# Optimization experiments

Measured on AMD Instinct MI355X. Metric: run time of the kernel, lower is better.

## Reference

```python
import jax, jax.numpy as jnp
import numpy as np

NSAMPLE = 16   # knn neighbors for cost volume
KCLUST = 8     # cluster size stand-in for custom_cluster_pc1 (min_count=8)
B, N, D = 2, 4096, 64


def _sqdist(src, dst):
    # src [B,N,C], dst [B,M,C] -> [B,N,M]
    d = (jnp.sum(src * src, -1)[:, :, None]
         + jnp.sum(dst * dst, -1)[:, None, :]
         - 2.0 * jnp.einsum('bnc,bmc->bnm', src, dst))
    return jnp.maximum(d, 0.0)


def _knn(k, xyz, new_xyz):
    return jax.lax.top_k(-_sqdist(new_xyz, xyz), k)[1]  # [B,S,k] indices of k smallest


def _group(points, idx):
    # points [B,M,C], idx [B,N,K] -> [B,N,K,C]
    b = jnp.arange(points.shape[0])[:, None, None]
    return points[b, idx]


def _weightnet(x, w1, b1, w2, b2, w3, b3):
    # x [B,N,K,3]; 1x1 conv stack == per-point MLP, relu
    h = jax.nn.relu(jnp.einsum('bnkc,cd->bnkd', x, w1) + b1)
    h = jax.nn.relu(jnp.einsum('bnkc,cd->bnkd', h, w2) + b2)
    return jax.nn.relu(jnp.einsum('bnkc,cd->bnkd', h, w3) + b3)


def _leaky(x):
    return jnp.where(x > 0, x, 0.1 * x)


def _forward(xyz1, xyz2, points1, points2, vel1, vel2, mask1, mask2,
             w_xyz, w_vel, w_points,
             mlp_w1, mlp_b1, mlp_w2, mlp_b2,
             wn1_w1, wn1_b1, wn1_w2, wn1_b2, wn1_w3, wn1_b3,
             wn2_w1, wn2_b1, wn2_w2, wn2_b2, wn2_w3, wn2_b3):
    xyz1t = jnp.transpose(xyz1, (0, 2, 1))      # [B,N1,3]
    xyz2t = jnp.transpose(xyz2, (0, 2, 1))      # [B,N2,3]
    p1t = jnp.transpose(points1, (0, 2, 1))     # [B,N1,D1]
    p2t = jnp.transpose(points2, (0, 2, 1))     # [B,N2,D2]

    # --- custom_cluster_pc1 stand-in: knn clusters of pc1 with its velocities ---
    idx_c = _knn(KCLUST, xyz1t, xyz1t)                     # [B,N,KC]
    cc = _group(xyz1t, idx_c)                              # [B,N,KC,3]
    cv = _group(vel1[..., None], idx_c)[..., 0]            # [B,N,KC]

    u = cc / jnp.linalg.norm(cc, axis=-1, keepdims=True)
    ATA = jnp.einsum('bnki,bnkj->bnij', u, u) + 1e-6 * jnp.eye(3, dtype=u.dtype)
    ATb = jnp.einsum('bnki,bnk->bni', u, cv)
    v_world = jnp.linalg.solve(ATA, ATb[..., None])[..., 0]  # [B,N,3]

    # --- feature-space knn between weighted (xyz, points) concatenations ---
    f1 = jnp.concatenate([w_xyz * xyz1t, w_points * p1t], axis=-1)
    f2 = jnp.concatenate([w_xyz * xyz2t, w_points * p2t], axis=-1)
    knn_idx = _knn(NSAMPLE, f2, f1)                        # [B,N1,K]

    neighbor_xyz = _group(xyz2t, knn_idx)                  # [B,N1,K,3]
    direction_xyz = neighbor_xyz - xyz1t[:, :, None, :]
    g2 = _group(p2t, knn_idx)                              # [B,N1,K,D2]
    g1 = jnp.broadcast_to(p1t[:, :, None, :], g2.shape[:3] + (p1t.shape[-1],))
    new_points = jnp.concatenate([g1, g2, direction_xyz], axis=-1)  # [B,N1,K,D1+D2+3]

    h = _leaky(jnp.einsum('bnkc,cd->bnkd', new_points, mlp_w1) + mlp_b1)
    h = _leaky(jnp.einsum('bnkc,cd->bnkd', h, mlp_w2) + mlp_b2)    # [B,N1,K,128]

    w = _weightnet(direction_xyz, wn1_w1, wn1_b1, wn1_w2, wn1_b2, wn1_w3, wn1_b3)
    point_to_patch = jnp.sum(w * h, axis=2)                # [B,N1,128]

    # --- second grouping in rigid-velocity space ---
    idx2 = _knn(NSAMPLE, v_world, v_world)
    nxyz1 = _group(xyz1t, idx2)
    dir2 = nxyz1 - xyz1t[:, :, None, :]
    w2 = _weightnet(dir2, wn2_w1, wn2_b1, wn2_w2, wn2_b2, wn2_w3, wn2_b3)
    gcost = _group(point_to_patch, idx2)                   # [B,N1,K,128]
    patch_to_patch = jnp.sum(w2 * gcost, axis=2)           # [B,N1,128]

    return jnp.transpose(patch_to_patch, (0, 2, 1)), v_world  # [B,128,N1], [B,N1,3]


def setup_inputs() -> dict:
    key = jax.random.key(0)
    ks = jax.random.split(key, 24)
    s = 0.05
    inp = {
        'xyz1': jax.random.normal(ks[0], (B, 3, N), jnp.float32),
        'xyz2': jax.random.normal(ks[1], (B, 3, N), jnp.float32),
        'points1': jax.random.normal(ks[2], (B, D, N), jnp.float32),
        'points2': jax.random.normal(ks[3], (B, D, N), jnp.float32),
        'vel1': jax.random.normal(ks[4], (B, N), jnp.float32),
        'vel2': jax.random.normal(ks[5], (B, N), jnp.float32),
        'mask1': jnp.ones((B, N), jnp.float32),
        'mask2': jnp.ones((B, N), jnp.float32),
        'w_xyz': jnp.float32(0.4), 'w_vel': jnp.float32(0.2), 'w_points': jnp.float32(0.4),
        'mlp_w1': jax.random.normal(ks[6], (2 * D + 3, 128), jnp.float32) * s,
        'mlp_b1': jnp.zeros((128,), jnp.float32),
        'mlp_w2': jax.random.normal(ks[7], (128, 128), jnp.float32) * s,
        'mlp_b2': jnp.zeros((128,), jnp.float32),
    }
    for tag, base in (('wn1', 8), ('wn2', 14)):
        inp[f'{tag}_w1'] = jax.random.normal(ks[base], (3, 8), jnp.float32) * s
        inp[f'{tag}_b1'] = jnp.zeros((8,), jnp.float32)
        inp[f'{tag}_w2'] = jax.random.normal(ks[base + 1], (8, 8), jnp.float32) * s
        inp[f'{tag}_b2'] = jnp.zeros((8,), jnp.float32)
        inp[f'{tag}_w3'] = jax.random.normal(ks[base + 2], (8, 128), jnp.float32) * s
        inp[f'{tag}_b3'] = jnp.zeros((128,), jnp.float32)
    return inp


def reference(xyz1, xyz2, points1, points2, vel1, vel2, mask1, mask2,
              w_xyz, w_vel, w_points,
              mlp_w1, mlp_b1, mlp_w2, mlp_b2,
              wn1_w1, wn1_b1, wn1_w2, wn1_b2, wn1_w3, wn1_b3,
              wn2_w1, wn2_b1, wn2_w2, wn2_b2, wn2_w3, wn2_b3):
    return _forward(xyz1, xyz2, points1, points2, vel1, vel2, mask1, mask2,
                    w_xyz, w_vel, w_points,
                    mlp_w1, mlp_b1, mlp_w2, mlp_b2,
                    wn1_w1, wn1_b1, wn1_w2, wn1_b2, wn1_w3, wn1_b3,
                    wn2_w1, wn2_b1, wn2_w2, wn2_b2, wn2_w3, wn2_b3)
```

## Files before the change

### kernel.cpp

```cpp
#include <hip/hip_runtime.h>

#define NPTS 4096
#define NQ   8192
#define DD   64
#define KNN  16
#define KC   8
#define NSEG3 32
#define NPSEG 32
#define KB96 96
#define FSTR 104
#define VOFF 1048576

#define ALWAYS_INLINE __attribute__((always_inline)) inline

typedef __attribute__((ext_vector_type(8))) short bf16x8;
typedef __attribute__((ext_vector_type(4))) float f32x4;

__device__ ALWAYS_INLINE float leakyf(float x) { return x > 0.f ? x : 0.1f * x; }

__device__ ALWAYS_INLINE unsigned short bf16rne(float f) {
  unsigned u = __float_as_uint(f);
  u = (u + 0x7FFFu + ((u >> 16) & 1u)) >> 16;
  return (unsigned short)u;
}

__device__ ALWAYS_INLINE float packdt(float d, unsigned tag12) {
  return __uint_as_float((__float_as_uint(d) & 0xFFFFF000u) | tag12);
}

#define TK8_FOREACH(M)  M(0) M(1) M(2) M(3) M(4) M(5) M(6) M(7)
#define TK16_FOREACH(M) M(0) M(1) M(2) M(3) M(4) M(5) M(6) M(7) \
                        M(8) M(9) M(10) M(11) M(12) M(13) M(14) M(15)

#define TK_DECL1(i) float tkd##i = 3.4e38f; int tki##i = 0;
#define TK_STEP1(i) { bool c = vd < tkd##i; float t_ = tkd##i; int u_ = tki##i; \
                      tkd##i = c ? vd : tkd##i; tki##i = c ? vi : tki##i; \
                      vd = c ? t_ : vd; vi = c ? u_ : vi; }
#define TK8_DECL  TK8_FOREACH(TK_DECL1)
#define TK8_INS(dexp, mexp)  { float vd = (dexp); int vi = (mexp); \
                               if (vd < tkd7)  { TK8_FOREACH(TK_STEP1) } }
#define TK8_RESET1(i) tkd##i = 3.4e38f; tki##i = 0;

#define PK_DECL1(i) float pk##i = __uint_as_float(0x7F7FFFFFu);
#define PK_RESET1(i) pk##i = __uint_as_float(0x7F7FFFFFu);
#define PK_STEP1(i) { float lo_ = fminf(pk##i, pv); pv = fmaxf(pk##i, pv); pk##i = lo_; }
#define PK16_DECL    TK16_FOREACH(PK_DECL1)
#define PK16_INS(ve) { float pv = (ve); TK16_FOREACH(PK_STEP1) }
#define PK_STORE1(i) pdq[i] = pk##i;
#define PK16_STORE   TK16_FOREACH(PK_STORE1)

__global__ __launch_bounds__(256) void k_prep(
    const float* __restrict__ xyz1, const float* __restrict__ xyz2,
    const float* __restrict__ pts1, const float* __restrict__ pts2,
    const float* __restrict__ w_xyz_p, const float* __restrict__ w_points_p,
    unsigned short* __restrict__ f1b, unsigned short* __restrict__ f2b,
    float* __restrict__ n1, float* __restrict__ n2a,
    float* __restrict__ p1t, float* __restrict__ p2t,
    float* __restrict__ x1t, float* __restrict__ x2t)
{
  __shared__ float s_acc[64][5];
  int tid = threadIdx.x;
  int nl = tid & 63, part = tid >> 6;
  int cloud = blockIdx.x >> 7;
  int gid = ((blockIdx.x & 127) << 6) + nl;
  int b = gid >> 12, n = gid & (NPTS - 1);
  float wx = w_xyz_p[0], wp = w_points_p[0];
  const float* xyz = cloud ? xyz2 : xyz1;
  const float* pts = cloud ? pts2 : pts1;
  unsigned short* fb = cloud ? f2b : f1b;
  float* nrm = cloud ? n2a : n1;
  float* pt  = cloud ? p2t : p1t;
  float* xt  = cloud ? x2t : x1t;
  const float* pb = pts + (size_t)b * DD * NPTS;
  float* pr = pt + (size_t)gid * DD;
  unsigned short* fr = fb + (size_t)gid * KB96;
  int c0 = part * 16;
  float acc = 0.f;
#pragma unroll 4
  for (int j = 0; j < 16; ++j) {
    float v = pb[(size_t)(c0 + j) * NPTS + n];
    pr[c0 + j] = v;
    float fv = wp * v;
    fr[3 + c0 + j] = bf16rne(fv);
    acc = fmaf(fv, fv, acc);
  }
  s_acc[nl][part] = acc;
  if (part == 1) { for (int c = 67; c < 82; ++c) fr[c] = 0; }
  else if (part == 2) { for (int c = 82; c < KB96; ++c) fr[c] = 0; }
  __syncthreads();
  if (part == 0) {
    const float* xb = xyz + (size_t)b * 3 * NPTS;
    float x = xb[n], y = xb[NPTS + n], z = xb[2 * NPTS + n];
    float nrm2 = fmaf(z, z, fmaf(y, y, x * x));
    float4 xv; xv.x = x; xv.y = y; xv.z = z; xv.w = nrm2;
    *(float4*)&xt[(size_t)gid * 4] = xv;
    float fx = wx * x, fy = wx * y, fz = wx * z;
    fr[0] = bf16rne(fx); fr[1] = bf16rne(fy); fr[2] = bf16rne(fz);
    float a = fmaf(fz, fz, fmaf(fy, fy, fx * fx));
    a += s_acc[nl][0] + s_acc[nl][1] + s_acc[nl][2] + s_acc[nl][3];
    nrm[gid] = a;
  }
}

__global__ __launch_bounds__(256) void k_knn3(
    const float* __restrict__ x4, float* __restrict__ pd, int* __restrict__ pi)
{
  __shared__ __align__(16) float4 sc[128];
  int seg = blockIdx.y;
  int Q = blockIdx.x * 256 + threadIdx.x;
  int b = Q >> 12;
  float4 q = *(const float4*)&x4[(size_t)Q * 4];
  TK8_DECL
  int gbase = (b << 12) + seg * 128;
  if (threadIdx.x < 128)
    sc[threadIdx.x] = *(const float4*)&x4[(size_t)(gbase + threadIdx.x) * 4];
  __syncthreads();
  int m0 = seg * 128;
#pragma unroll
  for (int j = 0; j < 128; ++j) {
    float4 c = sc[j];
    float dot = fmaf(q.z, c.z, fmaf(q.y, c.y, q.x * c.x));
    float d = fmaxf(q.w + c.w - 2.f * dot, 0.f);
    TK8_INS(d, m0 + j)
  }
  float* pdq = pd + ((size_t)Q * NSEG3 + seg) * 8;
  int* piq = pi + ((size_t)Q * NSEG3 + seg) * 8;
#define ST8(i) pdq[i] = tkd##i; piq[i] = tki##i;
  TK8_FOREACH(ST8)
#undef ST8
}

__global__ __launch_bounds__(256) void k_knnv(
    const float* __restrict__ x4, float* __restrict__ pd)
{
  __shared__ __align__(16) float4 sc[128];
  int seg = blockIdx.y;
  int Q = blockIdx.x * 256 + threadIdx.x;
  int b = Q >> 12;
  float4 q = *(const float4*)&x4[(size_t)Q * 4];
  PK16_DECL
  int gbase = (b << 12) + seg * 128;
  if (threadIdx.x < 128)
    sc[threadIdx.x] = *(const float4*)&x4[(size_t)(gbase + threadIdx.x) * 4];
  __syncthreads();
#pragma unroll
  for (int j = 0; j < 128; ++j) {
    float4 c = sc[j];
    float dot = fmaf(q.z, c.z, fmaf(q.y, c.y, q.x * c.x));
    float d = fmaxf(q.w + c.w - 2.f * dot, 0.f);
    PK16_INS(packdt(d, ((unsigned)j << 5) | (unsigned)seg))
  }
  float* pdq = pd + ((size_t)Q * NPSEG + seg) * 16;
  PK16_STORE
}

__global__ __launch_bounds__(256) void k_rigid(
    const float* __restrict__ pd, const int* __restrict__ pi,
    const float* __restrict__ x4, const float* __restrict__ vel1,
    float* __restrict__ vout, float* __restrict__ v4out)
{
  __shared__ __align__(16) float s_d[64][33];
  __shared__ __align__(16) int   s_i[64][33];
  int tid = threadIdx.x;
  int ql = tid >> 2, part = tid & 3;
  int Q = blockIdx.x * 64 + ql;
  int b = Q >> 12;
  TK8_DECL
  {
    int s0 = part * 8;
    const float* pbase = pd + ((size_t)Q * NSEG3 + s0) * 8;
    const int* ibase = pi + ((size_t)Q * NSEG3 + s0) * 8;
#pragma unroll
    for (int s = 0; s < 8; ++s) {
#pragma unroll
      for (int j = 0; j < 8; ++j) TK8_INS(pbase[s * 8 + j], ibase[s * 8 + j])
    }
  }
#define STP(i) s_d[ql][part * 8 + i] = tkd##i; s_i[ql][part * 8 + i] = tki##i;
  TK8_FOREACH(STP)
#undef STP
  __syncthreads();
  if (part != 0) return;
  TK8_FOREACH(TK8_RESET1)
#pragma unroll
  for (int j = 0; j < 32; ++j) TK8_INS(s_d[ql][j], s_i[ql][j])
  int base = b << 12;
  double a00 = 0, a01 = 0, a02 = 0, a11 = 0, a12 = 0, a22 = 0;
  double r0 = 0, r1 = 0, r2 = 0;
#define RIG_ACC(i) { \
    float4 c = *(const float4*)&x4[(size_t)(base + tki##i) * 4]; \
    float nr = sqrtf(c.w); \
    float ux = c.x / nr, uy = c.y / nr, uz = c.z / nr; \
    float cv = vel1[base + tki##i]; \
    double dx = ux, dy = uy, dz = uz, dvv = cv; \
    a00 += dx * dx; a01 += dx * dy; a02 += dx * dz; \
    a11 += dy * dy; a12 += dy * dz; a22 += dz * dz; \
    r0 += dx * dvv; r1 += dy * dvv; r2 += dz * dvv; }
  TK8_FOREACH(RIG_ACC)
#undef RIG_ACC
  a00 += 1e-6; a11 += 1e-6; a22 += 1e-6;
  double c00 = a11 * a22 - a12 * a12;
  double c01 = a02 * a12 - a01 * a22;
  double c02 = a01 * a12 - a02 * a11;
  double c11 = a00 * a22 - a02 * a02;
  double c12 = a02 * a01 - a00 * a12;
  double c22 = a00 * a11 - a01 * a01;
  double det = a00 * c00 + a01 * c01 + a02 * c02;
  double inv = 1.0 / det;
  float vx = (float)((c00 * r0 + c01 * r1 + c02 * r2) * inv);
  float vy = (float)((c01 * r0 + c11 * r1 + c12 * r2) * inv);
  float vz = (float)((c02 * r0 + c12 * r1 + c22 * r2) * inv);
  vout[(size_t)Q * 3 + 0] = vx;
  vout[(size_t)Q * 3 + 1] = vy;
  vout[(size_t)Q * 3 + 2] = vz;
  float4 v; v.x = vx; v.y = vy; v.z = vz;
  v.w = fmaf(vz, vz, fmaf(vy, vy, vx * vx));
  *(float4*)&v4out[(size_t)Q * 4] = v;
}

__global__ __launch_bounds__(256) void k_knnf_mfma(
    const unsigned short* __restrict__ f1b, const unsigned short* __restrict__ f2b,
    const float* __restrict__ n1, const float* __restrict__ n2a,
    float* __restrict__ pd)
{
  __shared__ __align__(16) unsigned short sf1[16 * FSTR];
  __shared__ __align__(16) unsigned short sf2[2][64 * FSTR];
  __shared__ __align__(16) float sn1[16];
  __shared__ __align__(16) float sn2[2][64];
  __shared__ __align__(16) float sD[64][17];
  int tid = threadIdx.x;
  int w = tid >> 6, lane = tid & 63;
  int i15 = lane & 15, g = lane >> 4, kr0 = g * 8;
  int blockq = blockIdx.x * 16;
  int b = blockq >> 12;
  int seg = blockIdx.y;
  int gbase = (b << 12) + seg * 2048;
  {
    const float4* src = (const float4*)(f1b + (size_t)blockq * KB96);
    if (tid < 192) ((float4*)sf1)[tid + tid / 12] = src[tid];
    if (tid < 16) sn1[tid] = n1[blockq + tid];
  }
  {
    const float4* src = (const float4*)(f2b + (size_t)gbase * KB96);
    int i0 = tid, i1 = tid + 256, i2 = tid + 512;
    ((float4*)sf2[0])[i0 + i0 / 12] = src[i0];
    ((float4*)sf2[0])[i1 + i1 / 12] = src[i1];
    ((float4*)sf2[0])[i2 + i2 / 12] = src[i2];
    if (tid < 64) sn2[0][tid] = n2a[gbase + tid];
  }
  __syncthreads();
  bf16x8 af0 = *(const bf16x8*)&sf1[i15 * FSTR + kr0];
  bf16x8 af1 = *(const bf16x8*)&sf1[i15 * FSTR + 32 + kr0];
  bf16x8 af2 = *(const bf16x8*)&sf1[i15 * FSTR + 64 + kr0];
  float nq0 = sn1[g * 4 + 0], nq1 = sn1[g * 4 + 1];
  float nq2 = sn1[g * 4 + 2], nq3 = sn1[g * 4 + 3];
  PK16_DECL
  int q_tk = tid & 15, p_tk = tid >> 4;
  for (int ch = 0; ch < 32; ++ch) {
    int cur = ch & 1;
    {
      int crow = w * 16 + i15;
      const unsigned short* c_ = &sf2[cur][crow * FSTR + kr0];
      f32x4 acc = {0.f, 0.f, 0.f, 0.f};
      acc = __builtin_amdgcn_mfma_f32_16x16x32_bf16(af0, *(const bf16x8*)&c_[0],  acc, 0, 0, 0);
      acc = __builtin_amdgcn_mfma_f32_16x16x32_bf16(af1, *(const bf16x8*)&c_[32], acc, 0, 0, 0);
      acc = __builtin_amdgcn_mfma_f32_16x16x32_bf16(af2, *(const bf16x8*)&c_[64], acc, 0, 0, 0);
      float nn2 = sn2[cur][crow];
      unsigned tag = (((unsigned)(ch * 4 + (crow & 3))) << 5) |
                     (unsigned)(seg * 16 + (crow >> 2));
      sD[crow][g * 4 + 0] = packdt(fmaxf(nq0 + nn2 - 2.f * acc[0], 0.f), tag);
      sD[crow][g * 4 + 1] = packdt(fmaxf(nq1 + nn2 - 2.f * acc[1], 0.f), tag);
      sD[crow][g * 4 + 2] = packdt(fmaxf(nq2 + nn2 - 2.f * acc[2], 0.f), tag);
      sD[crow][g * 4 + 3] = packdt(fmaxf(nq3 + nn2 - 2.f * acc[3], 0.f), tag);
    }
    __syncthreads();
    if (ch + 1 < 32) {
      const float4* src = (const float4*)(f2b + (size_t)(gbase + (ch + 1) * 64) * KB96);
      int i0 = tid, i1 = tid + 256, i2 = tid + 512;
      ((float4*)sf2[cur ^ 1])[i0 + i0 / 12] = src[i0];
      ((float4*)sf2[cur ^ 1])[i1 + i1 / 12] = src[i1];
      ((float4*)sf2[cur ^ 1])[i2 + i2 / 12] = src[i2];
      if (tid < 64) sn2[cur ^ 1][tid] = n2a[gbase + (ch + 1) * 64 + tid];
    }
#pragma unroll
    for (int j = 0; j < 4; ++j)
      PK16_INS(sD[p_tk * 4 + j][q_tk])
    __syncthreads();
  }
  int pseg = seg * 16 + p_tk;
  float* pdq = pd + ((size_t)(blockq + q_tk) * NPSEG + pseg) * 16;
  PK16_STORE
}

template<int MODE>
__global__ __launch_bounds__(256) void k_mergepk(
    const float* __restrict__ pd, int* __restrict__ oidx)
{
  __shared__ __align__(16) float s_k[64][65];
  int tid = threadIdx.x;
  int ql = tid >> 2, part = tid & 3;
  int Q = blockIdx.x * 64 + ql;
  PK16_DECL
  {
    const float* pbase = pd + ((size_t)Q * NPSEG + part * 8) * 16;
#pragma unroll
    for (int s = 0; s < 8; ++s) {
      for (int j = 0; j < 16; ++j) {
        float v = pbase[s * 16 + j];
        if (!(v < pk15)) break;
        PK16_INS(v)
      }
    }
  }
#define STK(i) s_k[ql][part * 16 + i] = pk##i;
  TK16_FOREACH(STK)
#undef STK
  __syncthreads();
  if (part != 0) return;
  TK16_FOREACH(PK_RESET1)
#pragma unroll
  for (int p = 0; p < 4; ++p) {
    for (int j = 0; j < 16; ++j) {
      float v = s_k[ql][p * 16 + j];
      if (!(v < pk15)) break;
      PK16_INS(v)
    }
  }
#define DEC(i) { unsigned u = __float_as_uint(pk##i); int m_; \
    unsigned ps = u & 31u, lo = (u >> 5) & 127u; \
    if (MODE == 0) m_ = (int)(((ps >> 4) << 11) + ((lo >> 2) << 6) + ((ps & 15u) << 2) + (lo & 3u)); \
    else m_ = (int)((ps << 7) + lo); \
    oidx[(size_t)Q * KNN + i] = m_; }
  TK16_FOREACH(DEC)
#undef DEC
}

#define PPB 8
__device__ ALWAYS_INLINE bf16x8 load_wfrag(const float* __restrict__ Wg,
                                           int kbase, int col, int kmax) {
  bf16x8 r;
#pragma unroll
  for (int j = 0; j < 8; ++j) {
    int k = kbase + j;
    float f = (k < kmax) ? Wg[(size_t)k * 128 + col] : 0.f;
    r[j] = (short)bf16rne(f);
  }
  return r;
}

__global__ __launch_bounds__(512) void k_mlp_mfma(
    const float* __restrict__ p1t, const float* __restrict__ p2t,
    const float* __restrict__ x1t, const float* __restrict__ x2t,
    const int* __restrict__ kidx,
    const float* __restrict__ W1, const float* __restrict__ B1v,
    const float* __restrict__ W2, const float* __restrict__ B2v,
    const float* __restrict__ wnw1, const float* __restrict__ wnb1,
    const float* __restrict__ wnw2, const float* __restrict__ wnb2,
    const float* __restrict__ wnw3, const float* __restrict__ wnb3,
    float* __restrict__ ptp)
{
  __shared__ __align__(16) unsigned short sA1[16 * 168];
  __shared__ __align__(16) unsigned short sH1[16 * 136];
  __shared__ __align__(16) float s_wv[16 * 128];
  __shared__ __align__(16) float s_c1[24];
  __shared__ __align__(16) float s_cb1[8];
  __shared__ __align__(16) float s_c2[64];
  __shared__ __align__(16) float s_cb2[8];
  __shared__ __align__(16) float s_w3[1024];
  __shared__ __align__(16) float s_b3[128];
  int tid = threadIdx.x;
  int w = tid >> 6, lane = tid & 63;
  int col = (w << 4) + (lane & 15);
  int kr0 = (lane >> 4) * 8;
  if (tid < 24) s_c1[tid] = wnw1[tid];
  else if (tid < 32) s_cb1[tid - 24] = wnb1[tid - 24];
  else if (tid < 96) s_c2[tid - 32] = wnw2[tid - 32];
  else if (tid < 104) s_cb2[tid - 96] = wnb2[tid - 96];
  if (tid >= 128 && tid < 256) s_b3[tid - 128] = wnb3[tid - 128];
  for (int i = tid; i < 1024; i += 512) s_w3[i] = wnw3[i];
  bf16x8 w1f0 = load_wfrag(W1, 0 + kr0, col, 131);
  bf16x8 w1f1 = load_wfrag(W1, 32 + kr0, col, 131);
  bf16x8 w1f2 = load_wfrag(W1, 64 + kr0, col, 131);
  bf16x8 w1f3 = load_wfrag(W1, 96 + kr0, col, 131);
  bf16x8 w1f4 = load_wfrag(W1, 128 + kr0, col, 131);
  bf16x8 w2f0 = load_wfrag(W2, 0 + kr0, col, 128);
  bf16x8 w2f1 = load_wfrag(W2, 32 + kr0, col, 128);
  bf16x8 w2f2 = load_wfrag(W2, 64 + kr0, col, 128);
  bf16x8 w2f3 = load_wfrag(W2, 96 + kr0, col, 128);
  float b1c = B1v[col], b2c = B2v[col];
  int blk0 = blockIdx.x * PPB;
  int base = (blk0 >> 12) << 12;
  int r_st = tid >> 5, t_st = tid & 31;

  for (int p = 0; p < PPB; ++p) {
    int gid = blk0 + p;
    __syncthreads();
    {
      int m = kidx[(size_t)gid * 16 + r_st];
      int grow = base + m;
      float4 cx1 = *(const float4*)&x1t[(size_t)gid * 4];
      float4 cx2 = *(const float4*)&x2t[(size_t)grow * 4];
      unsigned short* row = &sA1[r_st * 168];
      row[t_st]      = bf16rne(p1t[(size_t)gid * 64 + t_st]);
      row[t_st + 32] = bf16rne(p1t[(size_t)gid * 64 + t_st + 32]);
      row[t_st + 64] = bf16rne(p2t[(size_t)grow * 64 + t_st]);
      row[t_st + 96] = bf16rne(p2t[(size_t)grow * 64 + t_st + 32]);
      float dx = cx2.x - cx1.x, dy = cx2.y - cx1.y, dz = cx2.z - cx1.z;
      float dv_ = (t_st == 0) ? dx : (t_st == 1) ? dy : (t_st == 2) ? dz : 0.f;
      row[t_st + 128] = bf16rne(dv_);
      float h1w0 = fmaxf(fmaf(dz, s_c1[16], fmaf(dy, s_c1[8],  fmaf(dx, s_c1[0], s_cb1[0]))), 0.f);
      float h1w1 = fmaxf(fmaf(dz, s_c1[17], fmaf(dy, s_c1[9],  fmaf(dx, s_c1[1], s_cb1[1]))), 0.f);
      float h1w2 = fmaxf(fmaf(dz, s_c1[18], fmaf(dy, s_c1[10], fmaf(dx, s_c1[2], s_cb1[2]))), 0.f);
      float h1w3 = fmaxf(fmaf(dz, s_c1[19], fmaf(dy, s_c1[11], fmaf(dx, s_c1[3], s_cb1[3]))), 0.f);
      float h1w4 = fmaxf(fmaf(dz, s_c1[20], fmaf(dy, s_c1[12], fmaf(dx, s_c1[4], s_cb1[4]))), 0.f);
      float h1w5 = fmaxf(fmaf(dz, s_c1[21], fmaf(dy, s_c1[13], fmaf(dx, s_c1[5], s_cb1[5]))), 0.f);
      float h1w6 = fmaxf(fmaf(dz, s_c1[22], fmaf(dy, s_c1[14], fmaf(dx, s_c1[6], s_cb1[6]))), 0.f);
      float h1w7 = fmaxf(fmaf(dz, s_c1[23], fmaf(dy, s_c1[15], fmaf(dx, s_c1[7], s_cb1[7]))), 0.f);
#define H2W(j) float h2w##j; { float a_ = s_cb2[j]; \
      a_ = fmaf(h1w0, s_c2[0 * 8 + j], a_); a_ = fmaf(h1w1, s_c2[1 * 8 + j], a_); \
      a_ = fmaf(h1w2, s_c2[2 * 8 + j], a_); a_ = fmaf(h1w3, s_c2[3 * 8 + j], a_); \
      a_ = fmaf(h1w4, s_c2[4 * 8 + j], a_); a_ = fmaf(h1w5, s_c2[5 * 8 + j], a_); \
      a_ = fmaf(h1w6, s_c2[6 * 8 + j], a_); a_ = fmaf(h1w7, s_c2[7 * 8 + j], a_); \
      h2w##j = fmaxf(a_, 0.f); }
      H2W(0) H2W(1) H2W(2) H2W(3) H2W(4) H2W(5) H2W(6) H2W(7)
#undef H2W
      int c4 = t_st * 4;
      float4 wv = *(const float4*)&s_b3[c4];
#define WV(j) { float4 w3 = *(const float4*)&s_w3[j * 128 + c4]; \
      wv.x = fmaf(h2w##j, w3.x, wv.x); wv.y = fmaf(h2w##j, w3.y, wv.y); \
      wv.z = fmaf(h2w##j, w3.z, wv.z); wv.w = fmaf(h2w##j, w3.w, wv.w); }
      WV(0) WV(1) WV(2) WV(3) WV(4) WV(5) WV(6) WV(7)
#undef WV
      wv.x = fmaxf(wv.x, 0.f); wv.y = fmaxf(wv.y, 0.f);
      wv.z = fmaxf(wv.z, 0.f); wv.w = fmaxf(wv.w, 0.f);
      *(float4*)&s_wv[r_st * 128 + c4] = wv;
    }
    __syncthreads();
    {
      int ab = (lane & 15) * 168 + kr0;
      f32x4 acc = {0.f, 0.f, 0.f, 0.f};
      acc = __builtin_amdgcn_mfma_f32_16x16x32_bf16(*(const bf16x8*)&sA1[ab],       w1f0, acc, 0, 0, 0);
      acc = __builtin_amdgcn_mfma_f32_16x16x32_bf16(*(const bf16x8*)&sA1[ab + 32],  w1f1, acc, 0, 0, 0);
      acc = __builtin_amdgcn_mfma_f32_16x16x32_bf16(*(const bf16x8*)&sA1[ab + 64],  w1f2, acc, 0, 0, 0);
      acc = __builtin_amdgcn_mfma_f32_16x16x32_bf16(*(const bf16x8*)&sA1[ab + 96],  w1f3, acc, 0, 0, 0);
      acc = __builtin_amdgcn_mfma_f32_16x16x32_bf16(*(const bf16x8*)&sA1[ab + 128], w1f4, acc, 0, 0, 0);
      int rw0 = (lane >> 4) * 4;
#pragma unroll
      for (int r = 0; r < 4; ++r)
        sH1[(rw0 + r) * 136 + col] = bf16rne(leakyf(acc[r] + b1c));
    }
    __syncthreads();
    {
      int ab = (lane & 15) * 136 + kr0;
      f32x4 acc = {0.f, 0.f, 0.f, 0.f};
      acc = __builtin_amdgcn_mfma_f32_16x16x32_bf16(*(const bf16x8*)&sH1[ab],      w2f0, acc, 0, 0, 0);
      acc = __builtin_amdgcn_mfma_f32_16x16x32_bf16(*(const bf16x8*)&sH1[ab + 32], w2f1, acc, 0, 0, 0);
      acc = __builtin_amdgcn_mfma_f32_16x16x32_bf16(*(const bf16x8*)&sH1[ab + 64], w2f2, acc, 0, 0, 0);
      acc = __builtin_amdgcn_mfma_f32_16x16x32_bf16(*(const bf16x8*)&sH1[ab + 96], w2f3, acc, 0, 0, 0);
      int rw0 = (lane >> 4) * 4;
      float v = 0.f;
#pragma unroll
      for (int r = 0; r < 4; ++r)
        v = fmaf(s_wv[(rw0 + r) * 128 + col], leakyf(acc[r] + b2c), v);
      v += __shfl_xor(v, 16);
      v += __shfl_xor(v, 32);
      if (lane < 16) ptp[(size_t)gid * 128 + col] = v;
    }
  }
}

__global__ __launch_bounds__(256) void k_final(
    const float* __restrict__ x1t, const int* __restrict__ idx2,
    const float* __restrict__ ptp,
    const float* __restrict__ wnw1, const float* __restrict__ wnb1,
    const float* __restrict__ wnw2, const float* __restrict__ wnb2,
    const float* __restrict__ wnw3, const float* __restrict__ wnb3,
    float* __restrict__ out0)
{
  __shared__ __align__(16) float s_gc[16][128];
  __shared__ __align__(16) float s_wn[16][8];
  __shared__ __align__(16) float s_red[2][128];
  int gid = blockIdx.x, b = gid >> 12, n = gid & (NPTS - 1);
  int tid = threadIdx.x;
  if (tid < 16) {
    int m = idx2[(size_t)gid * 16 + tid];
    float4 c2 = *(const float4*)&x1t[(size_t)((b << 12) + m) * 4];
    float4 c1 = *(const float4*)&x1t[(size_t)gid * 4];
    float dx = c2.x - c1.x, dy = c2.y - c1.y, dz = c2.z - c1.z;
    float h1w[8];
#pragma unroll
    for (int j = 0; j < 8; ++j)
      h1w[j] = fmaxf(fmaf(dz, wnw1[16 + j], fmaf(dy, wnw1[8 + j], fmaf(dx, wnw1[j], wnb1[j]))), 0.f);
#pragma unroll
    for (int j = 0; j < 8; ++j) {
      float a = wnb2[j];
#pragma unroll
      for (int qq = 0; qq < 8; ++qq) a = fmaf(h1w[qq], wnw2[qq * 8 + j], a);
      s_wn[tid][j] = fmaxf(a, 0.f);
    }
  }
  int k2 = tid >> 4, i2 = tid & 15;
  int mg = idx2[(size_t)gid * 16 + k2];
  const float* src = &ptp[(size_t)((b << 12) + mg) * 128 + i2 * 8];
  *(float4*)&s_gc[k2][i2 * 8] = *(const float4*)&src[0];
  *(float4*)&s_gc[k2][i2 * 8 + 4] = *(const float4*)&src[4];
  __syncthreads();
  int ch = tid & 127, kg2 = tid >> 7;
  float r = 0.f;
#pragma unroll
  for (int jj = 0; jj < 8; ++jj) {
    int k = kg2 * 8 + jj;
    float4 wa = *(const float4*)&s_wn[k][0];
    float4 wb = *(const float4*)&s_wn[k][4];
    float wv = wnb3[ch];
    wv = fmaf(wa.x, wnw3[ch], wv);
    wv = fmaf(wa.y, wnw3[128 + ch], wv);
    wv = fmaf(wa.z, wnw3[256 + ch], wv);
    wv = fmaf(wa.w, wnw3[384 + ch], wv);
    wv = fmaf(wb.x, wnw3[512 + ch], wv);
    wv = fmaf(wb.y, wnw3[640 + ch], wv);
    wv = fmaf(wb.z, wnw3[768 + ch], wv);
    wv = fmaf(wb.w, wnw3[896 + ch], wv);
    wv = fmaxf(wv, 0.f);
    r = fmaf(wv, s_gc[k][ch], r);
  }
  s_red[kg2][ch] = r;
  __syncthreads();
  if (tid < 128)
    out0[(size_t)(b * 128 + tid) * NPTS + n] = s_red[0][tid] + s_red[1][tid];
}

extern "C" void kernel_launch(void* const* d_in, const int* in_sizes, int n_in,
                              void* d_out, int out_size, void* d_ws, size_t ws_size,
                              hipStream_t stream) {
  (void)in_sizes; (void)n_in; (void)out_size; (void)ws_size;
  const float* xyz1   = (const float*)d_in[0];
  const float* xyz2   = (const float*)d_in[1];
  const float* pts1   = (const float*)d_in[2];
  const float* pts2   = (const float*)d_in[3];
  const float* vel1   = (const float*)d_in[4];
  const float* w_xyz  = (const float*)d_in[8];
  const float* w_pts  = (const float*)d_in[10];
  const float* mlp_w1 = (const float*)d_in[11];
  const float* mlp_b1 = (const float*)d_in[12];
  const float* mlp_w2 = (const float*)d_in[13];
  const float* mlp_b2 = (const float*)d_in[14];
  const float* wn1_w1 = (const float*)d_in[15];
  const float* wn1_b1 = (const float*)d_in[16];
  const float* wn1_w2 = (const float*)d_in[17];
  const float* wn1_b2 = (const float*)d_in[18];
  const float* wn1_w3 = (const float*)d_in[19];
  const float* wn1_b3 = (const float*)d_in[20];
  const float* wn2_w1 = (const float*)d_in[21];
  const float* wn2_b1 = (const float*)d_in[22];
  const float* wn2_w2 = (const float*)d_in[23];
  const float* wn2_b2 = (const float*)d_in[24];
  const float* wn2_w3 = (const float*)d_in[25];
  const float* wn2_b3 = (const float*)d_in[26];

  char* ws = (char*)d_ws;
  size_t off = 0;
  float* pd   = (float*)(ws + off); off += (size_t)NQ * NPSEG * 16 * 4;
  int*   pi   = (int*)(ws + off);   off += (size_t)NQ * NSEG3 * 8 * 4;
  unsigned short* f1b = (unsigned short*)(ws + off); off += (size_t)NQ * KB96 * 2;
  unsigned short* f2b = (unsigned short*)(ws + off); off += (size_t)NQ * KB96 * 2;
  float* n1   = (float*)(ws + off); off += (size_t)NQ * 4;
  float* n2a  = (float*)(ws + off); off += (size_t)NQ * 4;
  float* p1t  = (float*)(ws + off); off += (size_t)NQ * DD * 4;
  float* p2t  = (float*)(ws + off); off += (size_t)NQ * DD * 4;
  float* x1t  = (float*)(ws + off); off += (size_t)NQ * 4 * 4;
  float* x2t  = (float*)(ws + off); off += (size_t)NQ * 4 * 4;
  int*   kidx = (int*)(ws + off);   off += (size_t)NQ * KNN * 4;
  float* ptp  = (float*)(ws + off); off += (size_t)NQ * 128 * 4;
  int*   idx2 = (int*)(ws + off);   off += (size_t)NQ * KNN * 4;
  float* v4   = (float*)(ws + off); off += (size_t)NQ * 4 * 4;

  float* out0 = (float*)d_out;
  float* outv = (float*)d_out + VOFF;

  k_prep<<<256, 256, 0, stream>>>(xyz1, xyz2, pts1, pts2, w_xyz, w_pts,
                                  f1b, f2b, n1, n2a, p1t, p2t, x1t, x2t);
  k_knn3<<<dim3(32, NSEG3), 256, 0, stream>>>(x1t, pd, pi);
  k_rigid<<<128, 256, 0, stream>>>(pd, pi, x1t, vel1, outv, v4);
  k_knnf_mfma<<<dim3(NQ / 16, 2), 256, 0, stream>>>(f1b, f2b, n1, n2a, pd);
  k_mergepk<0><<<128, 256, 0, stream>>>(pd, kidx);
  k_mlp_mfma<<<NQ / PPB, 512, 0, stream>>>(p1t, p2t, x1t, x2t, kidx,
                                           mlp_w1, mlp_b1, mlp_w2, mlp_b2,
                                           wn1_w1, wn1_b1, wn1_w2, wn1_b2,
                                           wn1_w3, wn1_b3, ptp);
  k_knnv<<<dim3(32, 32), 256, 0, stream>>>(v4, pd);
  k_mergepk<1><<<128, 256, 0, stream>>>(pd, idx2);
  k_final<<<NQ, 256, 0, stream>>>(x1t, pd == nullptr ? nullptr : idx2, ptp,
                                  wn2_w1, wn2_b1, wn2_w2, wn2_b2, wn2_w3, wn2_b3, out0);
}
```

Before: 335.2 us.

## Split feature-kNN candidates into four segments and drop double buffering

The feature-space kNN kernel now launches four candidate segments per query block instead of two, halving each block's loop. It also replaces the double-buffered shared-memory staging with a single buffer loaded synchronously each chunk. The partial top-16 buffer grows to 64 segments per query, the tag encoding is re-packed for the new bit layout, and the merge kernel uses eight parts per query in feature mode. This trades more grid parallelism and lower LDS use for more partial results to write and merge, and for losing overlap of loads with compute.

```diff
diff --git a/kernel.cpp b/kernel.cpp
--- a/kernel.cpp
+++ b/kernel.cpp
@@ -6,7 +6,8 @@
 #define KNN  16
 #define KC   8
 #define NSEG3 32
-#define NPSEG 32
+#define NPSF 64
+#define NPSV 32
 #define KB96 96
 #define FSTR 104
 #define VOFF 1048576
@@ -150,7 +151,7 @@
     float d = fmaxf(q.w + c.w - 2.f * dot, 0.f);
     PK16_INS(packdt(d, ((unsigned)j << 5) | (unsigned)seg))
   }
-  float* pdq = pd + ((size_t)Q * NPSEG + seg) * 16;
+  float* pdq = pd + ((size_t)Q * NPSV + seg) * 16;
   PK16_STORE
 }
 
@@ -224,9 +225,9 @@
     float* __restrict__ pd)
 {
   __shared__ __align__(16) unsigned short sf1[16 * FSTR];
-  __shared__ __align__(16) unsigned short sf2[2][64 * FSTR];
+  __shared__ __align__(16) unsigned short sf2[64 * FSTR];
   __shared__ __align__(16) float sn1[16];
-  __shared__ __align__(16) float sn2[2][64];
+  __shared__ __align__(16) float sn2[64];
   __shared__ __align__(16) float sD[64][17];
   int tid = threadIdx.x;
   int w = tid >> 6, lane = tid & 63;
@@ -234,19 +235,11 @@
   int blockq = blockIdx.x * 16;
   int b = blockq >> 12;
   int seg = blockIdx.y;
-  int gbase = (b << 12) + seg * 2048;
+  int gbase = (b << 12) + seg * 1024;
   {
     const float4* src = (const float4*)(f1b + (size_t)blockq * KB96);
     if (tid < 192) ((float4*)sf1)[tid + tid / 12] = src[tid];
     if (tid < 16) sn1[tid] = n1[blockq + tid];
-  }
-  {
-    const float4* src = (const float4*)(f2b + (size_t)gbase * KB96);
-    int i0 = tid, i1 = tid + 256, i2 = tid + 512;
-    ((float4*)sf2[0])[i0 + i0 / 12] = src[i0];
-    ((float4*)sf2[0])[i1 + i1 / 12] = src[i1];
-    ((float4*)sf2[0])[i2 + i2 / 12] = src[i2];
-    if (tid < 64) sn2[0][tid] = n2a[gbase + tid];
   }
   __syncthreads();
   bf16x8 af0 = *(const bf16x8*)&sf1[i15 * FSTR + kr0];
@@ -256,17 +249,26 @@
   float nq2 = sn1[g * 4 + 2], nq3 = sn1[g * 4 + 3];
   PK16_DECL
   int q_tk = tid & 15, p_tk = tid >> 4;
-  for (int ch = 0; ch < 32; ++ch) {
-    int cur = ch & 1;
+  for (int ch = 0; ch < 16; ++ch) {
+    __syncthreads();
+    {
+      const float4* src = (const float4*)(f2b + (size_t)(gbase + ch * 64) * KB96);
+      int i0 = tid, i1 = tid + 256, i2 = tid + 512;
+      ((float4*)sf2)[i0 + i0 / 12] = src[i0];
+      ((float4*)sf2)[i1 + i1 / 12] = src[i1];
+      ((float4*)sf2)[i2 + i2 / 12] = src[i2];
+      if (tid < 64) sn2[tid] = n2a[gbase + ch * 64 + tid];
+    }
+    __syncthreads();
     {
       int crow = w * 16 + i15;
-      const unsigned short* c_ = &sf2[cur][crow * FSTR + kr0];
+      const unsigned short* c_ = &sf2[crow * FSTR + kr0];
       f32x4 acc = {0.f, 0.f, 0.f, 0.f};
       acc = __builtin_amdgcn_mfma_f32_16x16x32_bf16(af0, *(const bf16x8*)&c_[0],  acc, 0, 0, 0);
       acc = __builtin_amdgcn_mfma_f32_16x16x32_bf16(af1, *(const bf16x8*)&c_[32], acc, 0, 0, 0);
       acc = __builtin_amdgcn_mfma_f32_16x16x32_bf16(af2, *(const bf16x8*)&c_[64], acc, 0, 0, 0);
-      float nn2 = sn2[cur][crow];
-      unsigned tag = (((unsigned)(ch * 4 + (crow & 3))) << 5) |
+      float nn2 = sn2[crow];
+      unsigned tag = (((unsigned)(ch * 4 + (crow & 3))) << 6) |
                      (unsigned)(seg * 16 + (crow >> 2));
       sD[crow][g * 4 + 0] = packdt(fmaxf(nq0 + nn2 - 2.f * acc[0], 0.f), tag);
       sD[crow][g * 4 + 1] = packdt(fmaxf(nq1 + nn2 - 2.f * acc[1], 0.f), tag);
@@ -274,21 +276,12 @@
       sD[crow][g * 4 + 3] = packdt(fmaxf(nq3 + nn2 - 2.f * acc[3], 0.f), tag);
     }
     __syncthreads();
-    if (ch + 1 < 32) {
-      const float4* src = (const float4*)(f2b + (size_t)(gbase + (ch + 1) * 64) * KB96);
-      int i0 = tid, i1 = tid + 256, i2 = tid + 512;
-      ((float4*)sf2[cur ^ 1])[i0 + i0 / 12] = src[i0];
-      ((float4*)sf2[cur ^ 1])[i1 + i1 / 12] = src[i1];
-      ((float4*)sf2[cur ^ 1])[i2 + i2 / 12] = src[i2];
-      if (tid < 64) sn2[cur ^ 1][tid] = n2a[gbase + (ch + 1) * 64 + tid];
-    }
 #pragma unroll
     for (int j = 0; j < 4; ++j)
       PK16_INS(sD[p_tk * 4 + j][q_tk])
-    __syncthreads();
   }
   int pseg = seg * 16 + p_tk;
-  float* pdq = pd + ((size_t)(blockq + q_tk) * NPSEG + pseg) * 16;
+  float* pdq = pd + ((size_t)(blockq + q_tk) * NPSF + pseg) * 16;
   PK16_STORE
 }
 
@@ -296,13 +289,16 @@
 __global__ __launch_bounds__(256) void k_mergepk(
     const float* __restrict__ pd, int* __restrict__ oidx)
 {
-  __shared__ __align__(16) float s_k[64][65];
+  constexpr int NPS = (MODE == 0) ? NPSF : NPSV;
+  constexpr int PARTS = (MODE == 0) ? 8 : 4;
+  constexpr int QPB = 256 / PARTS;
+  __shared__ __align__(16) float s_k[QPB][PARTS * 16 + 1];
   int tid = threadIdx.x;
-  int ql = tid >> 2, part = tid & 3;
-  int Q = blockIdx.x * 64 + ql;
+  int ql = tid / PARTS, part = tid % PARTS;
+  int Q = blockIdx.x * QPB + ql;
   PK16_DECL
   {
-    const float* pbase = pd + ((size_t)Q * NPSEG + part * 8) * 16;
+    const float* pbase = pd + ((size_t)Q * NPS + part * 8) * 16;
 #pragma unroll
     for (int s = 0; s < 8; ++s) {
       for (int j = 0; j < 16; ++j) {
@@ -319,7 +315,7 @@
   if (part != 0) return;
   TK16_FOREACH(PK_RESET1)
 #pragma unroll
-  for (int p = 0; p < 4; ++p) {
+  for (int p = 0; p < PARTS; ++p) {
     for (int j = 0; j < 16; ++j) {
       float v = s_k[ql][p * 16 + j];
       if (!(v < pk15)) break;
@@ -327,9 +323,9 @@
     }
   }
 #define DEC(i) { unsigned u = __float_as_uint(pk##i); int m_; \
-    unsigned ps = u & 31u, lo = (u >> 5) & 127u; \
-    if (MODE == 0) m_ = (int)(((ps >> 4) << 11) + ((lo >> 2) << 6) + ((ps & 15u) << 2) + (lo & 3u)); \
-    else m_ = (int)((ps << 7) + lo); \
+    if (MODE == 0) { unsigned ps = u & 63u, lo = (u >> 6) & 63u; \
+      m_ = (int)(((ps >> 4) << 10) + ((lo >> 2) << 6) + ((ps & 15u) << 2) + (lo & 3u)); } \
+    else { unsigned ps = u & 31u, lo = (u >> 5) & 127u; m_ = (int)((ps << 7) + lo); } \
     oidx[(size_t)Q * KNN + i] = m_; }
   TK16_FOREACH(DEC)
 #undef DEC
@@ -560,8 +556,8 @@
 
   char* ws = (char*)d_ws;
   size_t off = 0;
-  float* pd   = (float*)(ws + off); off += (size_t)NQ * NPSEG * 16 * 4;
-  int*   pi   = (int*)(ws + off);   off += (size_t)NQ * NSEG3 * 8 * 4;
+  float* pd   = (float*)(ws + off); off += (size_t)NQ * NPSF * 16 * 4;
+  int*   pi   = (int*)(pd + (size_t)NQ * NSEG3 * 8);
   unsigned short* f1b = (unsigned short*)(ws + off); off += (size_t)NQ * KB96 * 2;
   unsigned short* f2b = (unsigned short*)(ws + off); off += (size_t)NQ * KB96 * 2;
   float* n1   = (float*)(ws + off); off += (size_t)NQ * 4;
@@ -582,14 +578,14 @@
                                   f1b, f2b, n1, n2a, p1t, p2t, x1t, x2t);
   k_knn3<<<dim3(32, NSEG3), 256, 0, stream>>>(x1t, pd, pi);
   k_rigid<<<128, 256, 0, stream>>>(pd, pi, x1t, vel1, outv, v4);
-  k_knnf_mfma<<<dim3(NQ / 16, 2), 256, 0, stream>>>(f1b, f2b, n1, n2a, pd);
-  k_mergepk<0><<<128, 256, 0, stream>>>(pd, kidx);
+  k_knnf_mfma<<<dim3(NQ / 16, 4), 256, 0, stream>>>(f1b, f2b, n1, n2a, pd);
+  k_mergepk<0><<<NQ / 32, 256, 0, stream>>>(pd, kidx);
   k_mlp_mfma<<<NQ / PPB, 512, 0, stream>>>(p1t, p2t, x1t, x2t, kidx,
                                            mlp_w1, mlp_b1, mlp_w2, mlp_b2,
                                            wn1_w1, wn1_b1, wn1_w2, wn1_b2,
                                            wn1_w3, wn1_b3, ptp);
   k_knnv<<<dim3(32, 32), 256, 0, stream>>>(v4, pd);
-  k_mergepk<1><<<128, 256, 0, stream>>>(pd, idx2);
-  k_final<<<NQ, 256, 0, stream>>>(x1t, pd == nullptr ? nullptr : idx2, ptp,
+  k_mergepk<1><<<NQ / 64, 256, 0, stream>>>(pd, idx2);
+  k_final<<<NQ, 256, 0, stream>>>(x1t, idx2, ptp,
                                   wn2_w1, wn2_b1, wn2_w2, wn2_b2, wn2_w3, wn2_b3, out0);
 }
```

Result: slower. 351.7 us (+4.9%).
